# Kernel tuning notes

Measured on AMD Instinct MI355X. Metric: run time of the kernel, lower is better.

Reference implementation:

```python
import jax, jax.numpy as jnp
import numpy as np

N_NODES = 50000

def gcn_conv(x, src, dst, W, b, n_nodes):
    # PyG GCNConv: add self-loops, symmetric normalization D^-1/2 (A+I) D^-1/2, then bias
    loop = jnp.arange(n_nodes)
    s = jnp.concatenate([src, loop])
    d = jnp.concatenate([dst, loop])
    deg = jax.ops.segment_sum(jnp.ones(s.shape[0], x.dtype), d, num_segments=n_nodes)
    dinv = jnp.where(deg > 0, jax.lax.rsqrt(deg), 0.0)
    norm = dinv[s] * dinv[d]                      # [E+N]
    h = x @ W                                      # [N, out]
    msg = h[s] * norm[:, None]                     # gather + scale
    out = jax.ops.segment_sum(msg, d, num_segments=n_nodes)  # scatter-add
    return out + b

def setup_inputs() -> dict:
    key = jax.random.key(0)
    ks = jax.random.split(key, 8)
    x = jax.random.normal(ks[0], (N_NODES, 128), jnp.float32)
    edge_index = jax.random.randint(ks[1], (2, 800000), 0, N_NODES)
    def glorot(k, fan_in, fan_out):
        lim = np.sqrt(6.0 / (fan_in + fan_out)).astype(np.float32)
        return jax.random.uniform(k, (fan_in, fan_out), jnp.float32, -lim, lim)
    return {
        "x": x,
        "edge_index": edge_index,
        "conv_w1": glorot(ks[2], 128, 64), "conv_b1": jnp.zeros((64,), jnp.float32),
        "conv_w2": glorot(ks[3], 64, 64),  "conv_b2": jnp.zeros((64,), jnp.float32),
        "fc_w1": glorot(ks[4], 64, 32),    "fc_b1": jnp.zeros((32,), jnp.float32),
        "fc_w2": glorot(ks[5], 32, 1),     "fc_b2": jnp.zeros((1,), jnp.float32),
    }

def reference(x, edge_index, conv_w1, conv_b1, conv_w2, conv_b2, fc_w1, fc_b1, fc_w2, fc_b2):
    src, dst = edge_index[0], edge_index[1]
    h = jnp.tanh(gcn_conv(x, src, dst, conv_w1, conv_b1, N_NODES))
    h = jnp.tanh(gcn_conv(h, src, dst, conv_w2, conv_b2, N_NODES))
    h = jnp.tanh(h @ fc_w1 + fc_b1)  # dropout is identity at inference
    return h @ fc_w2 + fc_b2          # [N, 1]
```

## Files before the change

### kernel.cpp

```cpp
#include <hip/hip_runtime.h>
#include <math.h>

#define TPB 256
#define NBK_MAX 512
#define CAP 4096
#define FILL_CAP 4096
#define SC_CH 16
#define DMAX 64

typedef short bf16x8 __attribute__((ext_vector_type(8)));
typedef float f32x4 __attribute__((ext_vector_type(4)));

__device__ __forceinline__ unsigned short rne_bf16(float f) {
  unsigned u = __float_as_uint(f);
  return (unsigned short)((u + 0x7fffu + ((u >> 16) & 1u)) >> 16);
}
__device__ __forceinline__ float bf16_f(unsigned short v) {
  return __uint_as_float((unsigned)v << 16);
}
__device__ __forceinline__ float blo(unsigned u) { return __uint_as_float(u << 16); }
__device__ __forceinline__ float bhi(unsigned u) { return __uint_as_float(u & 0xffff0000u); }
__device__ __forceinline__ float ftanh(float x) {
  float xc = fminf(fmaxf(x, -15.f), 15.f);
  float e = __expf(2.f * xc);
  return (e - 1.f) * __builtin_amdgcn_rcpf(e + 1.f);
}

__global__ __launch_bounds__(TPB) void k_init(int* __restrict__ gcur,
                                              unsigned short* __restrict__ hz,
                                              int NBK, int N) {
  int i = blockIdx.x * TPB + threadIdx.x;
  if (i < NBK) gcur[i] = i * CAP;
  if (blockIdx.x == 0 && threadIdx.x < 32)
    ((unsigned*)(hz + ((size_t)N << 6)))[threadIdx.x] = 0;
}

__global__ __launch_bounds__(TPB) void k_bscatter(const int* __restrict__ src,
                                                  const int* __restrict__ dst,
                                                  int* __restrict__ gcur,
                                                  unsigned* __restrict__ e2,
                                                  int E, int NBK) {
  __shared__ int h[NBK_MAX];
  __shared__ int base[NBK_MAX];
  int tid = threadIdx.x, blk = blockIdx.x, G = gridDim.x;
  int chunk = (E + G - 1) / G, lo = blk * chunk, hi = min(E, lo + chunk);
  for (int t0 = lo; t0 < hi; t0 += TPB * SC_CH) {
    int sv[SC_CH], dv[SC_CH];
    for (int b = tid; b < NBK; b += TPB) h[b] = 0;
    __syncthreads();
#pragma unroll
    for (int u = 0; u < SC_CH; ++u) {
      int e = t0 + u * TPB + tid;
      if (e < hi) {
        dv[u] = dst[e];
        sv[u] = src[e];
        atomicAdd(&h[dv[u] >> 7], 1);
      } else {
        dv[u] = -1;
      }
    }
    __syncthreads();
    for (int b = tid; b < NBK; b += TPB) {
      int c = h[b];
      if (c) {
        int o = atomicAdd(&gcur[b], c);
        base[b] = min(o, (b + 1) * CAP - c);
      }
    }
    __syncthreads();
    for (int b = tid; b < NBK; b += TPB) h[b] = 0;
    __syncthreads();
#pragma unroll
    for (int u = 0; u < SC_CH; ++u) {
      if (dv[u] >= 0) {
        int bk = dv[u] >> 7;
        int r = atomicAdd(&h[bk], 1);
        e2[base[bk] + r] = ((unsigned)sv[u] << 7) | (unsigned)(dv[u] & 127);
      }
    }
    __syncthreads();
  }
}

__global__ __launch_bounds__(TPB) void k_build(const unsigned* __restrict__ e2,
                                               const int* __restrict__ gcur,
                                               float* __restrict__ dinv,
                                               unsigned short* __restrict__ col2, int N) {
  __shared__ int c[128], sc[128], cur[128];
  __shared__ int buf[FILL_CAP];
  int tid = threadIdx.x, b = blockIdx.x;
  int st = b * CAP;
  int en = min(gcur[b], st + FILL_CAP);
  if (tid < 128) c[tid] = 0;
  __syncthreads();
  for (int i = st + tid; i < en; i += TPB) atomicAdd(&c[e2[i] & 127u], 1);
  __syncthreads();
  if (tid < 128) sc[tid] = c[tid];
  __syncthreads();
  for (int o = 1; o < 128; o <<= 1) {
    int v = (tid >= o && tid < 128) ? sc[tid - o] : 0;
    __syncthreads();
    if (tid < 128) sc[tid] += v;
    __syncthreads();
  }
  if (tid < 128) {
    cur[tid] = sc[tid] - c[tid];
    int node = b * 128 + tid;
    if (node < N) dinv[node] = rsqrtf((float)(c[tid] + 1));
  }
  __syncthreads();
  for (int i = st + tid; i < en; i += TPB) {
    unsigned v = e2[i];
    int p = atomicAdd(&cur[v & 127u], 1);
    buf[p] = (int)(v >> 7);
  }
  __syncthreads();
  for (int i = tid; i < 128 * 32; i += TPB) {
    int nl = i >> 5, kk = i & 31;
    int node = b * 128 + nl;
    if (node < N) {
      int cc = c[nl], base0 = sc[nl] - cc;
      int k0 = kk * 2, k1 = kk * 2 + 1;
      unsigned v0 = (k0 == 0) ? (unsigned)node
                              : ((k0 - 1 < cc) ? (unsigned)buf[base0 + k0 - 1] : (unsigned)N);
      unsigned v1 = (k1 - 1 < cc) ? (unsigned)buf[base0 + k1 - 1] : (unsigned)N;
      ((unsigned*)col2)[((size_t)node << 5) + kk] = v0 | (v1 << 16);
    }
  }
}

template <int K, bool AF32>
__global__ __launch_bounds__(TPB) void k_mm(const void* __restrict__ Ap,
                                            const float* __restrict__ W,
                                            const float* __restrict__ dinv,
                                            unsigned short* __restrict__ Hout, int N) {
  constexpr int P = K + 8;
  __shared__ unsigned short sHi[64 * P];
  __shared__ unsigned short sLo[64 * P];
  int tid = threadIdx.x;
  for (int i = tid; i < K * 64; i += TPB) {
    int k = i >> 6, n = i & 63;
    float w = W[i];
    unsigned short hb = rne_bf16(w);
    sHi[n * P + k] = hb;
    sLo[n * P + k] = rne_bf16(w - bf16_f(hb));
  }
  __syncthreads();
  int wave = tid >> 6, lane = tid & 63;
  int oct = lane >> 4, l15 = lane & 15;
  int base = blockIdx.x * 64 + wave * 16;
  int arow = base + l15;
  if (arow >= N) arow = N - 1;
  f32x4 acc[4] = {};
#pragma unroll
  for (int s = 0; s < K / 32; ++s) {
    bf16x8 ahi, alo;
    if (AF32) {
      const float* ap = (const float*)Ap + (size_t)arow * K + s * 32 + oct * 8;
      float4 f0 = *(const float4*)ap;
      float4 f1 = *(const float4*)(ap + 4);
      float fv[8] = {f0.x, f0.y, f0.z, f0.w, f1.x, f1.y, f1.z, f1.w};
#pragma unroll
      for (int j = 0; j < 8; ++j) {
        unsigned short hb = rne_bf16(fv[j]);
        ahi[j] = (short)hb;
        alo[j] = (short)rne_bf16(fv[j] - bf16_f(hb));
      }
    } else {
      ahi = *(const bf16x8*)((const unsigned short*)Ap + (size_t)arow * K + s * 32 + oct * 8);
    }
#pragma unroll
    for (int t = 0; t < 4; ++t) {
      bf16x8 bh = *(const bf16x8*)(sHi + (t * 16 + l15) * P + s * 32 + oct * 8);
      bf16x8 bl = *(const bf16x8*)(sLo + (t * 16 + l15) * P + s * 32 + oct * 8);
      acc[t] = __builtin_amdgcn_mfma_f32_16x16x32_bf16(ahi, bh, acc[t], 0, 0, 0);
      acc[t] = __builtin_amdgcn_mfma_f32_16x16x32_bf16(ahi, bl, acc[t], 0, 0, 0);
      if (AF32)
        acc[t] = __builtin_amdgcn_mfma_f32_16x16x32_bf16(alo, bh, acc[t], 0, 0, 0);
    }
  }
#pragma unroll
  for (int r = 0; r < 4; ++r) {
    int row = base + oct * 4 + r;
    if (row < N) {
      float dv = dinv[row];
#pragma unroll
      for (int t = 0; t < 4; ++t)
        Hout[(size_t)row * 64 + t * 16 + l15] = rne_bf16(acc[t][r] * dv);
    }
  }
}


#define AQ_ISSUE(J, HVS)                                                        \
  {                                                                             \
    _Pragma("unroll") for (int g = 0; g < 8; ++g) {                             \
      int s0 = __builtin_amdgcn_readlane(sv[J], g);                             \
      int s1 = __builtin_amdgcn_readlane(sv[J], 8 + g);                         \
      unsigned off0 = ((unsigned)(half ? s1 : s0) << 7) + foff;                 \
      HVS[0][g] = *(const unsigned*)(Hb + off0);                                \
    }                                                                           \
    _Pragma("unroll") for (int g = 0; g < 8; ++g) {                             \
      int s0 = __builtin_amdgcn_readlane(sv[J], 16 + g);                        \
      int s1 = __builtin_amdgcn_readlane(sv[J], 24 + g);                        \
      unsigned off1 = ((unsigned)(half ? s1 : s0) << 7) + foff;                 \
      HVS[1][g] = *(const unsigned*)(Hb + off1);                                \
    }                                                                           \
  }

#define AQ_ACC(J, HVS)                                                          \
  {                                                                             \
    float x = 0.f, y = 0.f;                                                     \
    _Pragma("unroll") for (int g = 0; g < 8; ++g) {                             \
      x += blo(HVS[0][g]);                                                      \
      y += bhi(HVS[0][g]);                                                      \
    }                                                                           \
    _Pragma("unroll") for (int g = 0; g < 8; ++g) {                             \
      x += blo(HVS[1][g]);                                                      \
      y += bhi(HVS[1][g]);                                                      \
    }                                                                           \
    if (cnt[J] > 32) {                \
      for (int t = 32; t < cnt[J]; t += 16) {                                   \
        unsigned tv[8];                                                         \
        _Pragma("unroll") for (int g = 0; g < 8; ++g) {                         \
          int s0 = __builtin_amdgcn_readlane(sv[J], t + g);                     \
          int s1 = __builtin_amdgcn_readlane(sv[J], t + 8 + g);                 \
          unsigned offt = ((unsigned)(half ? s1 : s0) << 7) + foff;             \
          tv[g] = *(const unsigned*)(Hb + offt);                                \
        }                                                                       \
        _Pragma("unroll") for (int g = 0; g < 8; ++g) {                         \
          x += blo(tv[g]);                                                      \
          y += bhi(tv[g]);                                                      \
        }                                                                       \
      }                                                                         \
    }                                                                           \
    x += __shfl_xor(x, 32);                                                     \
    y += __shfl_xor(y, 32);                                                     \
    float di_ = rsqrtf((float)cnt[J]);                                          \
    float yx_ = ftanh(di_ * x + bf.x);                                          \
    float yy_ = ftanh(di_ * y + bf.y);                                          \
    if constexpr (DOFC) {                                                       \
      if (half == 0) {                                                          \
        float* sp_ = sA + ((wid << 3) + (J)) * 64 + f2 * 2;                     \
        sp_[0] = yx_;                                                           \
        sp_[1] = yy_;                                                           \
      }                                                                         \
    } else {                                                                    \
      if (half == 0 && qb + (J) < N) {                                          \
        unsigned pk_ = (unsigned)rne_bf16(yx_) | ((unsigned)rne_bf16(yy_) << 16); \
        ((unsigned*)OUT)[((size_t)(qb + (J)) << 5) + f2] = pk_;                 \
      }                                                                         \
    }                                                                           \
  }

template <bool DOFC>
__global__ __launch_bounds__(TPB) void k_agg(const unsigned short* __restrict__ H,
                                             const unsigned short* __restrict__ col2,
                                             const float* __restrict__ bias,
                                             unsigned short* __restrict__ OUT,
                                             const float* __restrict__ fw1,
                                             const float* __restrict__ fb1,
                                             const float* __restrict__ fw2,
                                             const float* __restrict__ fb2,
                                             float* __restrict__ fout, int N) {
  __shared__ float sw1t[DOFC ? 32 * 66 : 1];
  __shared__ float sb1[DOFC ? 32 : 1];
  __shared__ float sw2[DOFC ? 32 : 1];
  __shared__ float sA[DOFC ? 4 * 8 * 64 : 1];
  int tid = threadIdx.x;
  int wid = tid >> 6, lane = tid & 63;
  int f2 = lane & 31, half = lane >> 5;
  float b2v = 0.f;
  if constexpr (DOFC) {
    for (int i = tid; i < 32 * 64; i += TPB) {
      int j = i >> 6, k = i & 63;
      sw1t[j * 66 + k] = fw1[k * 32 + j];
    }
    if (tid < 32) { sb1[tid] = fb1[tid]; sw2[tid] = fw2[tid]; }
    b2v = fb2[0];
    __syncthreads();
  }
  float2 bf = *(const float2*)(bias + f2 * 2);
  const char* Hb = (const char*)H;
  unsigned foff = (unsigned)(f2 * 4);

  int qb = (blockIdx.x * 4 + wid) * 8;
  if (qb >= N) return;

  int idx[8];
#pragma unroll
  for (int j = 0; j < 8; ++j) idx[j] = min(qb + j, N - 1);
  int sv[8];
#pragma unroll
  for (int j = 0; j < 8; ++j) sv[j] = (int)col2[((size_t)idx[j] << 6) + lane];
  int cnt[8];
#pragma unroll
  for (int j = 0; j < 8; ++j) {
    unsigned long long mb_ = __ballot(sv[j] != N);
    cnt[j] = __builtin_amdgcn_readfirstlane((int)__popcll(mb_));
  }
  unsigned hvA[2][8], hvB[2][8];
  AQ_ISSUE(0, hvA)
  AQ_ISSUE(1, hvB)
  AQ_ACC(0, hvA)
  AQ_ISSUE(2, hvA)
  AQ_ACC(1, hvB)
  AQ_ISSUE(3, hvB)
  AQ_ACC(2, hvA)
  AQ_ISSUE(4, hvA)
  AQ_ACC(3, hvB)
  AQ_ISSUE(5, hvB)
  AQ_ACC(4, hvA)
  AQ_ISSUE(6, hvA)
  AQ_ACC(5, hvB)
  AQ_ISSUE(7, hvB)
  AQ_ACC(6, hvA)
  AQ_ACC(7, hvB)

  if constexpr (DOFC) {
    int m = lane & 31;
#pragma unroll
    for (int p = 0; p < 4; ++p) {
      int nl = p * 2 + half;
      int node = qb + nl;
      float acc = sb1[m];
      const float2* ar = (const float2*)(sA + ((wid << 3) + nl) * 64);
      const float2* wr = (const float2*)(sw1t + m * 66);
#pragma unroll
      for (int k2 = 0; k2 < 32; ++k2) {
        float2 av = ar[k2];
        float2 wv = wr[k2];
        acc += av.x * wv.x + av.y * wv.y;
      }
      float t = ftanh(acc) * sw2[m];
#pragma unroll
      for (int o = 1; o < 32; o <<= 1) t += __shfl_xor(t, o);
      if (m == 0 && node < N) fout[node] = t + b2v;
    }
  }
}


extern "C" void kernel_launch(void* const* d_in, const int* in_sizes, int n_in,
                              void* d_out, int out_size, void* d_ws, size_t ws_size,
                              hipStream_t stream) {
  const float* x   = (const float*)d_in[0];
  const int*   ei  = (const int*)d_in[1];
  const float* w1  = (const float*)d_in[2];
  const float* b1  = (const float*)d_in[3];
  const float* w2  = (const float*)d_in[4];
  const float* b2  = (const float*)d_in[5];
  const float* fw1 = (const float*)d_in[6];
  const float* fb1 = (const float*)d_in[7];
  const float* fw2 = (const float*)d_in[8];
  const float* fb2 = (const float*)d_in[9];
  float* out = (float*)d_out;

  int N = in_sizes[0] / 128;
  int E = in_sizes[1] / 2;
  const int* src = ei;
  const int* dst = ei + E;

  const int G   = 256;
  const int NBK = (N + 127) / 128;

  char* p = (char*)d_ws;
  size_t off = 0;
  auto take = [&](size_t bytes) -> void* {
    void* r = p + off;
    off += (bytes + 255) & ~(size_t)255;
    return r;
  };
  int*            gcur = (int*)take((size_t)NBK * 4);
  float*          dinv = (float*)take((size_t)N * 4);
  unsigned*       e2   = (unsigned*)take((size_t)NBK * CAP * 4);
  unsigned short* col2 = (unsigned short*)take((size_t)N * DMAX * 2);
  unsigned short* h    = (unsigned short*)take((size_t)(N + 1) * 64 * 2);
  unsigned short* a    = (unsigned short*)take((size_t)N * 64 * 2);
  (void)ws_size; (void)n_in; (void)out_size;

  k_init<<<(NBK + TPB - 1) / TPB, TPB, 0, stream>>>(gcur, h, NBK, N);
  k_bscatter<<<G, TPB, 0, stream>>>(src, dst, gcur, e2, E, NBK);
  k_build<<<NBK, TPB, 0, stream>>>(e2, gcur, dinv, col2, N);

  int gmm = (N + 63) / 64;
  int gagg = (N + 31) / 32;
  k_mm<128, true><<<gmm, TPB, 0, stream>>>(x, w1, dinv, h, N);
  k_agg<false><<<gagg, TPB, 0, stream>>>(h, col2, b1, a,
                                         nullptr, nullptr, nullptr, nullptr,
                                         nullptr, N);
  k_mm<64, false><<<gmm, TPB, 0, stream>>>(a, w2, dinv, h, N);
  k_agg<true><<<gagg, TPB, 0, stream>>>(h, col2, b2, nullptr,
                                        fw1, fb1, fw2, fb2, out, N);
}
```

Before: 183.1 us.

## Build padded adjacency directly with per-node global atomics

Drops the two-pass bucket scatter and per-bucket build, along with the e2 staging buffer. A fill kernel pre-initializes the padded col2 table with self-loop and sentinel entries and sets per-node counts to one. A single edge-scatter kernel then appends each source into its destination's row via a global atomic. Degree normalization becomes rsqrt of the count inside the matmul kernel. This removes a kernel launch and an intermediate pass, at the cost of many contended global atomics and scattered 2-byte writes. Neighbor order within each row also becomes nondeterministic.

```diff
diff --git a/kernel.cpp b/kernel.cpp
--- a/kernel.cpp
+++ b/kernel.cpp
@@ -2,10 +2,6 @@
 #include <math.h>
 
 #define TPB 256
-#define NBK_MAX 512
-#define CAP 4096
-#define FILL_CAP 4096
-#define SC_CH 16
 #define DMAX 64
 
 typedef short bf16x8 __attribute__((ext_vector_type(8)));
@@ -26,105 +22,44 @@
   return (e - 1.f) * __builtin_amdgcn_rcpf(e + 1.f);
 }
 
-__global__ __launch_bounds__(TPB) void k_init(int* __restrict__ gcur,
+__global__ __launch_bounds__(TPB) void k_fill(unsigned* __restrict__ col2w,
+                                              int* __restrict__ cnt,
                                               unsigned short* __restrict__ hz,
-                                              int NBK, int N) {
+                                              int N) {
   int i = blockIdx.x * TPB + threadIdx.x;
-  if (i < NBK) gcur[i] = i * CAP;
+  int total = N * 32;
+  if (i < total) {
+    int node = i >> 5, w = i & 31;
+    unsigned sent = (unsigned)N | ((unsigned)N << 16);
+    col2w[i] = (w == 0) ? ((unsigned)node | ((unsigned)N << 16)) : sent;
+    if (w == 0) cnt[node] = 1;
+  }
   if (blockIdx.x == 0 && threadIdx.x < 32)
     ((unsigned*)(hz + ((size_t)N << 6)))[threadIdx.x] = 0;
 }
 
-__global__ __launch_bounds__(TPB) void k_bscatter(const int* __restrict__ src,
+__global__ __launch_bounds__(TPB) void k_escatter(const int* __restrict__ src,
                                                   const int* __restrict__ dst,
-                                                  int* __restrict__ gcur,
-                                                  unsigned* __restrict__ e2,
-                                                  int E, int NBK) {
-  __shared__ int h[NBK_MAX];
-  __shared__ int base[NBK_MAX];
-  int tid = threadIdx.x, blk = blockIdx.x, G = gridDim.x;
-  int chunk = (E + G - 1) / G, lo = blk * chunk, hi = min(E, lo + chunk);
-  for (int t0 = lo; t0 < hi; t0 += TPB * SC_CH) {
-    int sv[SC_CH], dv[SC_CH];
-    for (int b = tid; b < NBK; b += TPB) h[b] = 0;
-    __syncthreads();
-#pragma unroll
-    for (int u = 0; u < SC_CH; ++u) {
-      int e = t0 + u * TPB + tid;
-      if (e < hi) {
-        dv[u] = dst[e];
-        sv[u] = src[e];
-        atomicAdd(&h[dv[u] >> 7], 1);
-      } else {
-        dv[u] = -1;
-      }
-    }
-    __syncthreads();
-    for (int b = tid; b < NBK; b += TPB) {
-      int c = h[b];
-      if (c) {
-        int o = atomicAdd(&gcur[b], c);
-        base[b] = min(o, (b + 1) * CAP - c);
-      }
-    }
-    __syncthreads();
-    for (int b = tid; b < NBK; b += TPB) h[b] = 0;
-    __syncthreads();
-#pragma unroll
-    for (int u = 0; u < SC_CH; ++u) {
-      if (dv[u] >= 0) {
-        int bk = dv[u] >> 7;
-        int r = atomicAdd(&h[bk], 1);
-        e2[base[bk] + r] = ((unsigned)sv[u] << 7) | (unsigned)(dv[u] & 127);
-      }
-    }
-    __syncthreads();
-  }
-}
-
-__global__ __launch_bounds__(TPB) void k_build(const unsigned* __restrict__ e2,
-                                               const int* __restrict__ gcur,
-                                               float* __restrict__ dinv,
-                                               unsigned short* __restrict__ col2, int N) {
-  __shared__ int c[128], sc[128], cur[128];
-  __shared__ int buf[FILL_CAP];
-  int tid = threadIdx.x, b = blockIdx.x;
-  int st = b * CAP;
-  int en = min(gcur[b], st + FILL_CAP);
-  if (tid < 128) c[tid] = 0;
-  __syncthreads();
-  for (int i = st + tid; i < en; i += TPB) atomicAdd(&c[e2[i] & 127u], 1);
-  __syncthreads();
-  if (tid < 128) sc[tid] = c[tid];
-  __syncthreads();
-  for (int o = 1; o < 128; o <<= 1) {
-    int v = (tid >= o && tid < 128) ? sc[tid - o] : 0;
-    __syncthreads();
-    if (tid < 128) sc[tid] += v;
-    __syncthreads();
-  }
-  if (tid < 128) {
-    cur[tid] = sc[tid] - c[tid];
-    int node = b * 128 + tid;
-    if (node < N) dinv[node] = rsqrtf((float)(c[tid] + 1));
-  }
-  __syncthreads();
-  for (int i = st + tid; i < en; i += TPB) {
-    unsigned v = e2[i];
-    int p = atomicAdd(&cur[v & 127u], 1);
-    buf[p] = (int)(v >> 7);
-  }
-  __syncthreads();
-  for (int i = tid; i < 128 * 32; i += TPB) {
-    int nl = i >> 5, kk = i & 31;
-    int node = b * 128 + nl;
-    if (node < N) {
-      int cc = c[nl], base0 = sc[nl] - cc;
-      int k0 = kk * 2, k1 = kk * 2 + 1;
-      unsigned v0 = (k0 == 0) ? (unsigned)node
-                              : ((k0 - 1 < cc) ? (unsigned)buf[base0 + k0 - 1] : (unsigned)N);
-      unsigned v1 = (k1 - 1 < cc) ? (unsigned)buf[base0 + k1 - 1] : (unsigned)N;
-      ((unsigned*)col2)[((size_t)node << 5) + kk] = v0 | (v1 << 16);
+                                                  int* __restrict__ cnt,
+                                                  unsigned short* __restrict__ col2,
+                                                  int E) {
+  int b0 = blockIdx.x * (TPB * 4) + threadIdx.x;
+  int dv[4], sv[4];
+#pragma unroll
+  for (int u = 0; u < 4; ++u) {
+    int e = b0 + u * TPB;
+    if (e < E) {
+      dv[u] = dst[e];
+      sv[u] = src[e];
+    } else {
+      dv[u] = -1;
+    }
+  }
+#pragma unroll
+  for (int u = 0; u < 4; ++u) {
+    if (dv[u] >= 0) {
+      int pos = atomicAdd(&cnt[dv[u]], 1);
+      if (pos < DMAX) col2[((size_t)dv[u] << 6) + pos] = (unsigned short)sv[u];
     }
   }
 }
@@ -132,7 +67,7 @@
 template <int K, bool AF32>
 __global__ __launch_bounds__(TPB) void k_mm(const void* __restrict__ Ap,
                                             const float* __restrict__ W,
-                                            const float* __restrict__ dinv,
+                                            const int* __restrict__ cnt,
                                             unsigned short* __restrict__ Hout, int N) {
   constexpr int P = K + 8;
   __shared__ unsigned short sHi[64 * P];
@@ -183,7 +118,7 @@
   for (int r = 0; r < 4; ++r) {
     int row = base + oct * 4 + r;
     if (row < N) {
-      float dv = dinv[row];
+      float dv = rsqrtf((float)cnt[row]);
 #pragma unroll
       for (int t = 0; t < 4; ++t)
         Hout[(size_t)row * 64 + t * 16 + l15] = rne_bf16(acc[t][r] * dv);
@@ -361,9 +296,6 @@
   const int* src = ei;
   const int* dst = ei + E;
 
-  const int G   = 256;
-  const int NBK = (N + 127) / 128;
-
   char* p = (char*)d_ws;
   size_t off = 0;
   auto take = [&](size_t bytes) -> void* {
@@ -371,25 +303,24 @@
     off += (bytes + 255) & ~(size_t)255;
     return r;
   };
-  int*            gcur = (int*)take((size_t)NBK * 4);
-  float*          dinv = (float*)take((size_t)N * 4);
-  unsigned*       e2   = (unsigned*)take((size_t)NBK * CAP * 4);
+  int*            cnt  = (int*)take((size_t)N * 4);
   unsigned short* col2 = (unsigned short*)take((size_t)N * DMAX * 2);
   unsigned short* h    = (unsigned short*)take((size_t)(N + 1) * 64 * 2);
   unsigned short* a    = (unsigned short*)take((size_t)N * 64 * 2);
   (void)ws_size; (void)n_in; (void)out_size;
 
-  k_init<<<(NBK + TPB - 1) / TPB, TPB, 0, stream>>>(gcur, h, NBK, N);
-  k_bscatter<<<G, TPB, 0, stream>>>(src, dst, gcur, e2, E, NBK);
-  k_build<<<NBK, TPB, 0, stream>>>(e2, gcur, dinv, col2, N);
+  int gfill = (N * 32 + TPB - 1) / TPB;
+  int gesc  = (E + TPB * 4 - 1) / (TPB * 4);
+  k_fill<<<gfill, TPB, 0, stream>>>((unsigned*)col2, cnt, h, N);
+  k_escatter<<<gesc, TPB, 0, stream>>>(src, dst, cnt, col2, E);
 
   int gmm = (N + 63) / 64;
   int gagg = (N + 31) / 32;
-  k_mm<128, true><<<gmm, TPB, 0, stream>>>(x, w1, dinv, h, N);
+  k_mm<128, true><<<gmm, TPB, 0, stream>>>(x, w1, cnt, h, N);
   k_agg<false><<<gagg, TPB, 0, stream>>>(h, col2, b1, a,
                                          nullptr, nullptr, nullptr, nullptr,
                                          nullptr, N);
-  k_mm<64, false><<<gmm, TPB, 0, stream>>>(a, w2, dinv, h, N);
+  k_mm<64, false><<<gmm, TPB, 0, stream>>>(a, w2, cnt, h, N);
   k_agg<true><<<gagg, TPB, 0, stream>>>(h, col2, b2, nullptr,
                                         fw1, fb1, fw2, fb2, out, N);
 }
```

Measured after the change: 212.6 us. 16.1% more time.

## Fuse layer-1 aggregation with layer-2 matmul into one MFMA kernel

Applied to the files above, without the earlier changes.

Merges the first aggregation kernel and the second dense matmul into one kernel, k_aggmm. Each wave aggregates 16 nodes into shared memory as bf16, then multiplies them by W2 using bf16 MFMA with a hi/lo split of W2 and scales by dinv. This removes one launch and the global write and re-read of the intermediate activation. In exchange it keeps two H buffers, uses more LDS per block (which may lower occupancy), and gives each wave more nodes, which raises register pressure.

```diff
diff --git a/kernel.cpp b/kernel.cpp
--- a/kernel.cpp
+++ b/kernel.cpp
@@ -27,12 +27,15 @@
 }
 
 __global__ __launch_bounds__(TPB) void k_init(int* __restrict__ gcur,
-                                              unsigned short* __restrict__ hz,
+                                              unsigned short* __restrict__ h1,
+                                              unsigned short* __restrict__ h2,
                                               int NBK, int N) {
   int i = blockIdx.x * TPB + threadIdx.x;
   if (i < NBK) gcur[i] = i * CAP;
-  if (blockIdx.x == 0 && threadIdx.x < 32)
-    ((unsigned*)(hz + ((size_t)N << 6)))[threadIdx.x] = 0;
+  if (blockIdx.x == 0 && threadIdx.x < 64) {
+    unsigned short* hz = (threadIdx.x < 32) ? h1 : h2;
+    ((unsigned*)(hz + ((size_t)N << 6)))[threadIdx.x & 31] = 0;
+  }
 }
 
 __global__ __launch_bounds__(TPB) void k_bscatter(const int* __restrict__ src,
@@ -208,82 +211,185 @@
     }                                                                           \
   }
 
-#define AQ_ACC(J, HVS)                                                          \
-  {                                                                             \
-    float x = 0.f, y = 0.f;                                                     \
-    _Pragma("unroll") for (int g = 0; g < 8; ++g) {                             \
-      x += blo(HVS[0][g]);                                                      \
-      y += bhi(HVS[0][g]);                                                      \
-    }                                                                           \
-    _Pragma("unroll") for (int g = 0; g < 8; ++g) {                             \
-      x += blo(HVS[1][g]);                                                      \
-      y += bhi(HVS[1][g]);                                                      \
-    }                                                                           \
-    if (cnt[J] > 32) {                \
-      for (int t = 32; t < cnt[J]; t += 16) {                                   \
-        unsigned tv[8];                                                         \
-        _Pragma("unroll") for (int g = 0; g < 8; ++g) {                         \
-          int s0 = __builtin_amdgcn_readlane(sv[J], t + g);                     \
-          int s1 = __builtin_amdgcn_readlane(sv[J], t + 8 + g);                 \
-          unsigned offt = ((unsigned)(half ? s1 : s0) << 7) + foff;             \
-          tv[g] = *(const unsigned*)(Hb + offt);                                \
-        }                                                                       \
-        _Pragma("unroll") for (int g = 0; g < 8; ++g) {                         \
-          x += blo(tv[g]);                                                      \
-          y += bhi(tv[g]);                                                      \
-        }                                                                       \
+#define AQ_SUM(J, HVS)                                                          \
+  float x = 0.f, y = 0.f;                                                       \
+  _Pragma("unroll") for (int g = 0; g < 8; ++g) {                               \
+    x += blo(HVS[0][g]);                                                        \
+    y += bhi(HVS[0][g]);                                                        \
+  }                                                                             \
+  _Pragma("unroll") for (int g = 0; g < 8; ++g) {                               \
+    x += blo(HVS[1][g]);                                                        \
+    y += bhi(HVS[1][g]);                                                        \
+  }                                                                             \
+  if (cnt[J] > 32) {                  \
+    for (int t = 32; t < cnt[J]; t += 16) {                                     \
+      unsigned tv[8];                                                           \
+      _Pragma("unroll") for (int g = 0; g < 8; ++g) {                           \
+        int s0 = __builtin_amdgcn_readlane(sv[J], t + g);                       \
+        int s1 = __builtin_amdgcn_readlane(sv[J], t + 8 + g);                   \
+        unsigned offt = ((unsigned)(half ? s1 : s0) << 7) + foff;               \
+        tv[g] = *(const unsigned*)(Hb + offt);                                  \
+      }                                                                         \
+      _Pragma("unroll") for (int g = 0; g < 8; ++g) {                           \
+        x += blo(tv[g]);                                                        \
+        y += bhi(tv[g]);                                                        \
       }                                                                         \
     }                                                                           \
-    x += __shfl_xor(x, 32);                                                     \
-    y += __shfl_xor(y, 32);                                                     \
-    float di_ = rsqrtf((float)cnt[J]);                                          \
-    float yx_ = ftanh(di_ * x + bf.x);                                          \
-    float yy_ = ftanh(di_ * y + bf.y);                                          \
-    if constexpr (DOFC) {                                                       \
-      if (half == 0) {                                                          \
-        float* sp_ = sA + ((wid << 3) + (J)) * 64 + f2 * 2;                     \
-        sp_[0] = yx_;                                                           \
-        sp_[1] = yy_;                                                           \
-      }                                                                         \
-    } else {                                                                    \
-      if (half == 0 && qb + (J) < N) {                                          \
-        unsigned pk_ = (unsigned)rne_bf16(yx_) | ((unsigned)rne_bf16(yy_) << 16); \
-        ((unsigned*)OUT)[((size_t)(qb + (J)) << 5) + f2] = pk_;                 \
-      }                                                                         \
+  }                                                                             \
+  x += __shfl_xor(x, 32);                                                       \
+  y += __shfl_xor(y, 32);                                                       \
+  float di_ = rsqrtf((float)cnt[J]);                                            \
+  float yx_ = ftanh(di_ * x + bf.x);                                            \
+  float yy_ = ftanh(di_ * y + bf.y);
+
+
+#define AM_ACC(J, HVS)                                                          \
+  {                                                                             \
+    AQ_SUM(J, HVS)                                                              \
+    if (half == 0) {                                                            \
+      unsigned pk_ = (unsigned)rne_bf16(yx_) | ((unsigned)rne_bf16(yy_) << 16); \
+      ((unsigned*)(sA2 + ((wid << 4) + (J)) * 72))[f2] = pk_;                   \
     }                                                                           \
-  }
-
-template <bool DOFC>
-__global__ __launch_bounds__(TPB) void k_agg(const unsigned short* __restrict__ H,
-                                             const unsigned short* __restrict__ col2,
-                                             const float* __restrict__ bias,
-                                             unsigned short* __restrict__ OUT,
-                                             const float* __restrict__ fw1,
-                                             const float* __restrict__ fb1,
-                                             const float* __restrict__ fw2,
-                                             const float* __restrict__ fb2,
-                                             float* __restrict__ fout, int N) {
-  __shared__ float sw1t[DOFC ? 32 * 66 : 1];
-  __shared__ float sb1[DOFC ? 32 : 1];
-  __shared__ float sw2[DOFC ? 32 : 1];
-  __shared__ float sA[DOFC ? 4 * 8 * 64 : 1];
+    if (lane == 0) sDi[(wid << 4) + (J)] = di_;                                 \
+  }
+
+__global__ __launch_bounds__(TPB) void k_aggmm(const unsigned short* __restrict__ H,
+                                               const unsigned short* __restrict__ col2,
+                                               const float* __restrict__ bias,
+                                               const float* __restrict__ W2,
+                                               unsigned short* __restrict__ Hout,
+                                               int N) {
+  __shared__ unsigned short sHi2[64 * 72];
+  __shared__ unsigned short sLo2[64 * 72];
+  __shared__ unsigned short sA2[4 * 16 * 72];
+  __shared__ float sDi[4 * 16];
   int tid = threadIdx.x;
   int wid = tid >> 6, lane = tid & 63;
   int f2 = lane & 31, half = lane >> 5;
-  float b2v = 0.f;
-  if constexpr (DOFC) {
-    for (int i = tid; i < 32 * 64; i += TPB) {
-      int j = i >> 6, k = i & 63;
-      sw1t[j * 66 + k] = fw1[k * 32 + j];
-    }
-    if (tid < 32) { sb1[tid] = fb1[tid]; sw2[tid] = fw2[tid]; }
-    b2v = fb2[0];
-    __syncthreads();
-  }
+  for (int i = tid; i < 64 * 64; i += TPB) {
+    int k = i >> 6, n = i & 63;
+    float w = W2[i];
+    unsigned short hb = rne_bf16(w);
+    sHi2[n * 72 + k] = hb;
+    sLo2[n * 72 + k] = rne_bf16(w - bf16_f(hb));
+  }
+  __syncthreads();
   float2 bf = *(const float2*)(bias + f2 * 2);
   const char* Hb = (const char*)H;
   unsigned foff = (unsigned)(f2 * 4);
 
+  int wqb = (blockIdx.x * 4 + wid) * 16;
+  if (wqb >= N) return;
+
+  int idx[16];
+#pragma unroll
+  for (int j = 0; j < 16; ++j) idx[j] = min(wqb + j, N - 1);
+  int sv[16];
+#pragma unroll
+  for (int j = 0; j < 16; ++j) sv[j] = (int)col2[((size_t)idx[j] << 6) + lane];
+  int cnt[16];
+#pragma unroll
+  for (int j = 0; j < 16; ++j) {
+    unsigned long long mb_ = __ballot(sv[j] != N);
+    cnt[j] = __builtin_amdgcn_readfirstlane((int)__popcll(mb_));
+  }
+  unsigned hvA[2][8], hvB[2][8];
+  AQ_ISSUE(0, hvA)
+  AQ_ISSUE(1, hvB)
+  AM_ACC(0, hvA)
+  AQ_ISSUE(2, hvA)
+  AM_ACC(1, hvB)
+  AQ_ISSUE(3, hvB)
+  AM_ACC(2, hvA)
+  AQ_ISSUE(4, hvA)
+  AM_ACC(3, hvB)
+  AQ_ISSUE(5, hvB)
+  AM_ACC(4, hvA)
+  AQ_ISSUE(6, hvA)
+  AM_ACC(5, hvB)
+  AQ_ISSUE(7, hvB)
+  AM_ACC(6, hvA)
+  AQ_ISSUE(8, hvA)
+  AM_ACC(7, hvB)
+  AQ_ISSUE(9, hvB)
+  AM_ACC(8, hvA)
+  AQ_ISSUE(10, hvA)
+  AM_ACC(9, hvB)
+  AQ_ISSUE(11, hvB)
+  AM_ACC(10, hvA)
+  AQ_ISSUE(12, hvA)
+  AM_ACC(11, hvB)
+  AQ_ISSUE(13, hvB)
+  AM_ACC(12, hvA)
+  AQ_ISSUE(14, hvA)
+  AM_ACC(13, hvB)
+  AQ_ISSUE(15, hvB)
+  AM_ACC(14, hvA)
+  AM_ACC(15, hvB)
+
+  int oct = lane >> 4, l15 = lane & 15;
+  f32x4 macc[4] = {};
+  const unsigned short* aRow = sA2 + ((wid << 4) + l15) * 72;
+#pragma unroll
+  for (int s = 0; s < 2; ++s) {
+    bf16x8 ahi = *(const bf16x8*)(aRow + s * 32 + oct * 8);
+#pragma unroll
+    for (int t = 0; t < 4; ++t) {
+      bf16x8 bh = *(const bf16x8*)(sHi2 + (t * 16 + l15) * 72 + s * 32 + oct * 8);
+      bf16x8 bl = *(const bf16x8*)(sLo2 + (t * 16 + l15) * 72 + s * 32 + oct * 8);
+      macc[t] = __builtin_amdgcn_mfma_f32_16x16x32_bf16(ahi, bh, macc[t], 0, 0, 0);
+      macc[t] = __builtin_amdgcn_mfma_f32_16x16x32_bf16(ahi, bl, macc[t], 0, 0, 0);
+    }
+  }
+#pragma unroll
+  for (int r = 0; r < 4; ++r) {
+    int row = oct * 4 + r;
+    int node = wqb + row;
+    if (node < N) {
+      float dvv = sDi[(wid << 4) + row];
+#pragma unroll
+      for (int t = 0; t < 4; ++t)
+        Hout[((size_t)node << 6) + t * 16 + l15] = rne_bf16(macc[t][r] * dvv);
+    }
+  }
+}
+
+#define AG_ACC(J, HVS)                                                          \
+  {                                                                             \
+    AQ_SUM(J, HVS)                                                              \
+    if (half == 0) {                                                            \
+      float* sp_ = sA + ((wid << 3) + (J)) * 64 + f2 * 2;                       \
+      sp_[0] = yx_;                                                             \
+      sp_[1] = yy_;                                                             \
+    }                                                                           \
+  }
+
+__global__ __launch_bounds__(TPB) void k_aggfc(const unsigned short* __restrict__ H,
+                                               const unsigned short* __restrict__ col2,
+                                               const float* __restrict__ bias,
+                                               const float* __restrict__ fw1,
+                                               const float* __restrict__ fb1,
+                                               const float* __restrict__ fw2,
+                                               const float* __restrict__ fb2,
+                                               float* __restrict__ fout, int N) {
+  __shared__ float sw1t[32 * 66];
+  __shared__ float sb1[32];
+  __shared__ float sw2[32];
+  __shared__ float sA[4 * 8 * 64];
+  int tid = threadIdx.x;
+  int wid = tid >> 6, lane = tid & 63;
+  int f2 = lane & 31, half = lane >> 5;
+  for (int i = tid; i < 32 * 64; i += TPB) {
+    int j = i >> 6, k = i & 63;
+    sw1t[j * 66 + k] = fw1[k * 32 + j];
+  }
+  if (tid < 32) { sb1[tid] = fb1[tid]; sw2[tid] = fw2[tid]; }
+  float b2v = fb2[0];
+  __syncthreads();
+  float2 bf = *(const float2*)(bias + f2 * 2);
+  const char* Hb = (const char*)H;
+  unsigned foff = (unsigned)(f2 * 4);
+
   int qb = (blockIdx.x * 4 + wid) * 8;
   if (qb >= N) return;
 
@@ -302,41 +408,39 @@
   unsigned hvA[2][8], hvB[2][8];
   AQ_ISSUE(0, hvA)
   AQ_ISSUE(1, hvB)
-  AQ_ACC(0, hvA)
+  AG_ACC(0, hvA)
   AQ_ISSUE(2, hvA)
-  AQ_ACC(1, hvB)
+  AG_ACC(1, hvB)
   AQ_ISSUE(3, hvB)
-  AQ_ACC(2, hvA)
+  AG_ACC(2, hvA)
   AQ_ISSUE(4, hvA)
-  AQ_ACC(3, hvB)
+  AG_ACC(3, hvB)
   AQ_ISSUE(5, hvB)
-  AQ_ACC(4, hvA)
+  AG_ACC(4, hvA)
   AQ_ISSUE(6, hvA)
-  AQ_ACC(5, hvB)
+  AG_ACC(5, hvB)
   AQ_ISSUE(7, hvB)
-  AQ_ACC(6, hvA)
-  AQ_ACC(7, hvB)
-
-  if constexpr (DOFC) {
-    int m = lane & 31;
-#pragma unroll
-    for (int p = 0; p < 4; ++p) {
-      int nl = p * 2 + half;
-      int node = qb + nl;
-      float acc = sb1[m];
-      const float2* ar = (const float2*)(sA + ((wid << 3) + nl) * 64);
-      const float2* wr = (const float2*)(sw1t + m * 66);
-#pragma unroll
-      for (int k2 = 0; k2 < 32; ++k2) {
-        float2 av = ar[k2];
-        float2 wv = wr[k2];
-        acc += av.x * wv.x + av.y * wv.y;
-      }
-      float t = ftanh(acc) * sw2[m];
-#pragma unroll
-      for (int o = 1; o < 32; o <<= 1) t += __shfl_xor(t, o);
-      if (m == 0 && node < N) fout[node] = t + b2v;
-    }
+  AG_ACC(6, hvA)
+  AG_ACC(7, hvB)
+
+  int m = lane & 31;
+#pragma unroll
+  for (int p = 0; p < 4; ++p) {
+    int nl = p * 2 + half;
+    int node = qb + nl;
+    float acc = sb1[m];
+    const float2* ar = (const float2*)(sA + ((wid << 3) + nl) * 64);
+    const float2* wr = (const float2*)(sw1t + m * 66);
+#pragma unroll
+    for (int k2 = 0; k2 < 32; ++k2) {
+      float2 av = ar[k2];
+      float2 wv = wr[k2];
+      acc += av.x * wv.x + av.y * wv.y;
+    }
+    float t = ftanh(acc) * sw2[m];
+#pragma unroll
+    for (int o = 1; o < 32; o <<= 1) t += __shfl_xor(t, o);
+    if (m == 0 && node < N) fout[node] = t + b2v;
   }
 }
 
@@ -375,21 +479,18 @@
   float*          dinv = (float*)take((size_t)N * 4);
   unsigned*       e2   = (unsigned*)take((size_t)NBK * CAP * 4);
   unsigned short* col2 = (unsigned short*)take((size_t)N * DMAX * 2);
-  unsigned short* h    = (unsigned short*)take((size_t)(N + 1) * 64 * 2);
-  unsigned short* a    = (unsigned short*)take((size_t)N * 64 * 2);
+  unsigned short* h1   = (unsigned short*)take((size_t)(N + 1) * 64 * 2);
+  unsigned short* h2   = (unsigned short*)take((size_t)(N + 1) * 64 * 2);
   (void)ws_size; (void)n_in; (void)out_size;
 
-  k_init<<<(NBK + TPB - 1) / TPB, TPB, 0, stream>>>(gcur, h, NBK, N);
+  k_init<<<(NBK + TPB - 1) / TPB, TPB, 0, stream>>>(gcur, h1, h2, NBK, N);
   k_bscatter<<<G, TPB, 0, stream>>>(src, dst, gcur, e2, E, NBK);
   k_build<<<NBK, TPB, 0, stream>>>(e2, gcur, dinv, col2, N);
 
-  int gmm = (N + 63) / 64;
+  int gmm  = (N + 63) / 64;
+  int gam  = (N + 63) / 64;
   int gagg = (N + 31) / 32;
-  k_mm<128, true><<<gmm, TPB, 0, stream>>>(x, w1, dinv, h, N);
-  k_agg<false><<<gagg, TPB, 0, stream>>>(h, col2, b1, a,
-                                         nullptr, nullptr, nullptr, nullptr,
-                                         nullptr, N);
-  k_mm<64, false><<<gmm, TPB, 0, stream>>>(a, w2, dinv, h, N);
-  k_agg<true><<<gagg, TPB, 0, stream>>>(h, col2, b2, nullptr,
-                                        fw1, fb1, fw2, fb2, out, N);
-}
+  k_mm<128, true><<<gmm, TPB, 0, stream>>>(x, w1, dinv, h1, N);
+  k_aggmm<<<gam, TPB, 0, stream>>>(h1, col2, b1, w2, h2, N);
+  k_aggfc<<<gagg, TPB, 0, stream>>>(h2, col2, b2, fw1, fb1, fw2, fb2, out, N);
+}
```

Measured after the change: 178.2 us. 1.03x faster.
